# Kernel optimization log

Hardware: AMD Instinct MI355X
Metric: run time of the kernel (lower is better)

## Reference

```python
import jax, jax.numpy as jnp
import numpy as np


def hard_sigmoid(x):
    # Keras/Theano hard_sigmoid: clip(0.2*x + 0.5, 0, 1)
    return jnp.clip(0.2 * x + 0.5, 0.0, 1.0)


def _lstm_scan(x, Wi, Ui, bi, Wf, Uf, bf, Wc, Uc, bc, Wo, Uo, bo):
    # x: [B, T, D]. Precompute input-to-gate projections as big GEMMs -> [T, B, H]
    xi = jnp.einsum('btd,dh->tbh', x, Wi) + bi
    xf = jnp.einsum('btd,dh->tbh', x, Wf) + bf
    xc = jnp.einsum('btd,dh->tbh', x, Wc) + bc
    xo = jnp.einsum('btd,dh->tbh', x, Wo) + bo

    B = x.shape[0]
    H = Ui.shape[0]
    h0 = jnp.zeros((B, H), dtype=x.dtype)
    c0 = jnp.zeros((B, H), dtype=x.dtype)

    def step(carry, gates):
        h, c = carry
        gi, gf, go, gc = gates
        i_t = hard_sigmoid(gi + h @ Ui)
        f_t = hard_sigmoid(gf + h @ Uf)
        o_t = hard_sigmoid(go + h @ Uo)
        g_t = jnp.tanh(gc + h @ Uc)
        c_t = f_t * c + i_t * g_t
        h_t = o_t * jnp.tanh(c_t)
        return (h_t, c_t), h_t

    _, hs = jax.lax.scan(step, (h0, c0), (xi, xf, xo, xc))  # hs: [T, B, H]
    return hs.transpose(1, 0, 2)  # [B, T, H]


def _bidir_lstm(x,
                W_i, U_i, b_i, W_f, U_f, b_f, W_c, U_c, b_c, W_o, U_o, b_o,
                Wb_i, Ub_i, bb_i, Wb_f, Ub_f, bb_f, Wb_c, Ub_c, bb_c, Wb_o, Ub_o, bb_o):
    forward = _lstm_scan(x, W_i, U_i, b_i, W_f, U_f, b_f, W_c, U_c, b_c, W_o, U_o, b_o)
    # Theano scan(go_backwards=True) iterates the reversed sequence and stacks
    # outputs in iteration order WITHOUT re-reversing; replicate by flipping x
    # in time and not flipping the scan output back.
    backward = _lstm_scan(x[:, ::-1, :], Wb_i, Ub_i, bb_i, Wb_f, Ub_f, bb_f,
                          Wb_c, Ub_c, bb_c, Wb_o, Ub_o, bb_o)
    # output_mode == 'sum', return_sequences == True
    return forward + backward  # [B, T, H]


def setup_inputs() -> dict:
    B, T, D, H = 32, 512, 512, 512
    key = jax.random.key(0)
    keys = jax.random.split(key, 17)
    x = jax.random.normal(keys[0], (B, T, D), dtype=jnp.float32)
    s_w = 1.0 / np.sqrt(D)   # glorot-ish for input weights
    s_u = 1.0 / np.sqrt(H)   # orthogonal-ish scale for recurrent weights
    names = ['W_i', 'W_f', 'W_c', 'W_o', 'Wb_i', 'Wb_f', 'Wb_c', 'Wb_o']
    unames = ['U_i', 'U_f', 'U_c', 'U_o', 'Ub_i', 'Ub_f', 'Ub_c', 'Ub_o']
    inp = {'x': x}
    for j, n in enumerate(names):
        inp[n] = jax.random.normal(keys[1 + j], (D, H), dtype=jnp.float32) * s_w
    for j, n in enumerate(unames):
        inp[n] = jax.random.normal(keys[9 + j], (H, H), dtype=jnp.float32) * s_u
    for n in ['b_i', 'b_f', 'b_c', 'b_o', 'bb_i', 'bb_f', 'bb_c', 'bb_o']:
        inp[n] = jnp.zeros((H,), dtype=jnp.float32)
    return inp


def reference(x,
              W_i, U_i, b_i, W_f, U_f, b_f, W_c, U_c, b_c, W_o, U_o, b_o,
              Wb_i, Ub_i, bb_i, Wb_f, Ub_f, bb_f, Wb_c, Ub_c, bb_c, Wb_o, Ub_o, bb_o):
    return _bidir_lstm(x,
                       W_i, U_i, b_i, W_f, U_f, b_f, W_c, U_c, b_c, W_o, U_o, b_o,
                       Wb_i, Ub_i, bb_i, Wb_f, Ub_f, bb_f, Wb_c, Ub_c, bb_c,
                       Wb_o, Ub_o, bb_o)
```

## Files before the change

kernel.cpp:

```cpp
#include <hip/hip_runtime.h>

typedef _Float16 half8 __attribute__((ext_vector_type(8)));
typedef float f32x4 __attribute__((ext_vector_type(4)));

#define TT 512
#define HH 512

#define OFF_HPK   16777216
#define OFF_FLAGS 50331648
#define OFF_UPK   50339840
#define OFF_WPK   54534144

struct BiasPtrs { const float* b[8]; };

struct PackParams {
  const float* U[8];
  const float* W[8];
  _Float16* Upk;
  _Float16* Wpk;
};

__global__ void convert_x_kernel(const float* __restrict__ x, _Float16* __restrict__ x16) {
  const size_t i = ((size_t)blockIdx.x * blockDim.x + threadIdx.x) * 8;
  float4 v0 = *(const float4*)(x + i);
  float4 v1 = *(const float4*)(x + i + 4);
  half8 h;
  h[0] = (_Float16)v0.x; h[1] = (_Float16)v0.y; h[2] = (_Float16)v0.z; h[3] = (_Float16)v0.w;
  h[4] = (_Float16)v1.x; h[5] = (_Float16)v1.y; h[6] = (_Float16)v1.z; h[7] = (_Float16)v1.w;
  *(half8*)(x16 + i) = h;
}

__global__ void pack_frags_kernel(PackParams p) {
  const unsigned n = blockIdx.x * 256 + threadIdx.x;
  const unsigned o = n & 2097151u;
  const int sel = n >> 21;
  const int jj = o & 7, l = (o >> 3) & 63, kt = (o >> 9) & 15;
  const int ct = (o >> 13) & 1, j = (o >> 14) & 63, d = (o >> 20) & 1;
  const int r15 = l & 15, kg = l >> 4;
  const int g = r15 & 3;
  const int u = j * 8 + ct * 4 + (r15 >> 2);
  const int k = kt * 32 + kg * 8 + jj;
  const float* M = sel ? p.W[4 * d + g] : p.U[4 * d + g];
  _Float16* dst = sel ? p.Wpk : p.Upk;
  dst[o] = (_Float16)M[k * HH + u];
}

__global__ void zero_flags_kernel(int* __restrict__ p) {
  __hip_atomic_store(p + blockIdx.x * 256 + threadIdx.x, 0,
                     __ATOMIC_RELAXED, __HIP_MEMORY_SCOPE_AGENT);
}

__device__ __forceinline__ float hsig(float x) {
  return fminf(fmaxf(fmaf(x, 0.2f, 0.5f), 0.0f), 1.0f);
}

__device__ __forceinline__ float fast_tanh(float x) {
  const float e = __expf(2.0f * x);
  return fmaf(-2.0f, __builtin_amdgcn_rcpf(e + 1.0f), 1.0f);
}

__global__ __launch_bounds__(256, 1) void lstm_scan_kernel(
    const _Float16* __restrict__ x16,
    _Float16* __restrict__ h_pk,
    int* __restrict__ flags,
    const _Float16* __restrict__ Upk,
    const _Float16* __restrict__ Wpk,
    BiasPtrs bp) {
  const int tid = threadIdx.x;
  const int bid = blockIdx.x;
  const int d   = bid & 1;
  const int j   = bid >> 1;
  const int w   = tid >> 6;
  const int l   = tid & 63;
  const int r15 = l & 15;
  const int kg  = l >> 4;
  const int rt  = w & 1;
  const int ct  = w >> 1;
  const int arow = rt * 16 + r15;

  __shared__ __align__(16) half8 ulds[2 * 16 * 64];
  __shared__ __align__(16) half8 wlds[2 * 16 * 64];
  __shared__ __align__(16) float zlds[32 * 36];
  __shared__ __align__(16) unsigned short hlds[256];

  {
    const half8* ub = (const half8*)Upk;
    const half8* wb = (const half8*)Wpk;
    const int base = (((d * 64 + j) * 2 + ct) * 16) * 64 + l;
    if (rt == 0) {
#pragma unroll
      for (int kt = 0; kt < 16; ++kt) {
        ulds[(ct * 16 + kt) * 64 + l] = ub[base + kt * 64];
        wlds[(ct * 16 + kt) * 64 + l] = wb[base + kt * 64];
      }
    }
  }

  const int b_e  = tid >> 3;
  const int uu_e = tid & 7;
  const int u_e  = j * 8 + uu_e;
  const int slot_e = (uu_e >> 2) * 16 + (uu_e & 3) * 4;
  f32x4 biasv;
#pragma unroll
  for (int g = 0; g < 4; ++g) biasv[g] = bp.b[4 * d + g][u_e];

  __syncthreads();

  float c = 0.0f;

  for (int s = 0; s < TT; ++s) {
    const int t = d ? (TT - 1 - s) : s;

    half8 xa[16];
    {
      const half8* xb = (const half8*)(x16 + ((size_t)arow * TT + t) * HH);
#pragma unroll
      for (int kt = 0; kt < 16; ++kt) xa[kt] = xb[kt * 4 + kg];
    }
    __builtin_amdgcn_sched_barrier(0);

    if (s > 0) {
      if (tid < 64) {
        const int* fl = flags + ((d * 8 + ((s - 1) & 7)) << 6) + tid;
        while (__hip_atomic_load(fl, __ATOMIC_RELAXED, __HIP_MEMORY_SCOPE_AGENT) < s) {
          __builtin_amdgcn_s_sleep(1);
        }
      }
      __syncthreads();
    }
    __builtin_amdgcn_sched_barrier(0);

    half8 ha[16];
    if (s > 0) {
      const half8* hb = (const half8*)(h_pk + (size_t)(d * TT + (s - 1)) * 16384);
#pragma unroll
      for (int kt = 0; kt < 16; ++kt) ha[kt] = hb[(kt * 4 + kg) * 32 + arow];
    }
    __builtin_amdgcn_sched_barrier(0);

    f32x4 acc0 = {0,0,0,0}, acc1 = {0,0,0,0}, acc2 = {0,0,0,0}, acc3 = {0,0,0,0};
#pragma unroll
    for (int kt = 0; kt < 16; ++kt) {
      const half8 wk = wlds[(ct * 16 + kt) * 64 + l];
      if ((kt & 3) == 0)      acc0 = __builtin_amdgcn_mfma_f32_16x16x32_f16(xa[kt], wk, acc0, 0, 0, 0);
      else if ((kt & 3) == 1) acc1 = __builtin_amdgcn_mfma_f32_16x16x32_f16(xa[kt], wk, acc1, 0, 0, 0);
      else if ((kt & 3) == 2) acc2 = __builtin_amdgcn_mfma_f32_16x16x32_f16(xa[kt], wk, acc2, 0, 0, 0);
      else                    acc3 = __builtin_amdgcn_mfma_f32_16x16x32_f16(xa[kt], wk, acc3, 0, 0, 0);
    }
    __builtin_amdgcn_sched_barrier(0);

    if (s > 0) {
#pragma unroll
      for (int kt = 0; kt < 16; ++kt) {
        const half8 uk = ulds[(ct * 16 + kt) * 64 + l];
        if ((kt & 3) == 0)      acc0 = __builtin_amdgcn_mfma_f32_16x16x32_f16(ha[kt], uk, acc0, 0, 0, 0);
        else if ((kt & 3) == 1) acc1 = __builtin_amdgcn_mfma_f32_16x16x32_f16(ha[kt], uk, acc1, 0, 0, 0);
        else if ((kt & 3) == 2) acc2 = __builtin_amdgcn_mfma_f32_16x16x32_f16(ha[kt], uk, acc2, 0, 0, 0);
        else                    acc3 = __builtin_amdgcn_mfma_f32_16x16x32_f16(ha[kt], uk, acc3, 0, 0, 0);
      }
    }
    const f32x4 z = (acc0 + acc1) + (acc2 + acc3);

#pragma unroll
    for (int i = 0; i < 4; ++i)
      zlds[(rt * 16 + kg * 4 + i) * 36 + ct * 16 + r15] = z[i];
    __syncthreads();

    f32x4 pre = *(const f32x4*)&zlds[(size_t)b_e * 36 + slot_e] + biasv;
    const float ig = hsig(pre[0]);
    const float fg = hsig(pre[1]);
    const float gg = fast_tanh(pre[2]);
    const float og = hsig(pre[3]);
    c = fg * c + ig * gg;
    const float h = og * fast_tanh(c);

    hlds[tid] = __builtin_bit_cast(unsigned short, (_Float16)h);
    __syncthreads();

    if (tid < 64) {
      const unsigned long long v = ((const unsigned long long*)hlds)[tid];
      unsigned long long* dst = (unsigned long long*)h_pk +
                                ((size_t)(d * TT + s) * 64 + j) * 64 + tid;
      __hip_atomic_store(dst, v, __ATOMIC_RELAXED, __HIP_MEMORY_SCOPE_AGENT);
      asm volatile("s_waitcnt vmcnt(0)" ::: "memory");
      if (tid == 0)
        __hip_atomic_store(flags + ((d * 8 + (s & 7)) << 6) + j, s + 1,
                           __ATOMIC_RELAXED, __HIP_MEMORY_SCOPE_AGENT);
    }
  }
}

__global__ void sum_out_kernel(const _Float16* __restrict__ h_pk, float* __restrict__ out) {
  const unsigned idx = blockIdx.x * 256 + threadIdx.x;
  const int j = idx & 63;
  const int t = (idx >> 6) & 511;
  const int b = idx >> 15;
  half8 hf = ((const half8*)h_pk)[((size_t)t * 64 + j) * 32 + b];
  half8 hg = ((const half8*)h_pk)[((size_t)(TT + t) * 64 + j) * 32 + b];
  float* o = out + (((size_t)b * TT + t) * HH + j * 8);
  float4 r0, r1;
  r0.x = (float)hf[0] + (float)hg[0]; r0.y = (float)hf[1] + (float)hg[1];
  r0.z = (float)hf[2] + (float)hg[2]; r0.w = (float)hf[3] + (float)hg[3];
  r1.x = (float)hf[4] + (float)hg[4]; r1.y = (float)hf[5] + (float)hg[5];
  r1.z = (float)hf[6] + (float)hg[6]; r1.w = (float)hf[7] + (float)hg[7];
  *(float4*)o = r0;
  *(float4*)(o + 4) = r1;
}

extern "C" void kernel_launch(void* const* d_in, const int* in_sizes, int n_in,
                              void* d_out, int out_size, void* d_ws, size_t ws_size,
                              hipStream_t stream) {
  (void)in_sizes; (void)n_in; (void)out_size; (void)ws_size;
  char* ws = (char*)d_ws;
  _Float16* x16   = (_Float16*)ws;
  _Float16* h_pk  = (_Float16*)(ws + OFF_HPK);
  int*      flags = (int*)(ws + OFF_FLAGS);
  _Float16* Upk   = (_Float16*)(ws + OFF_UPK);
  _Float16* Wpk   = (_Float16*)(ws + OFF_WPK);

  convert_x_kernel<<<4096, 256, 0, stream>>>((const float*)d_in[0], x16);

  PackParams pp;
  for (int g = 0; g < 8; ++g) {
    pp.W[g] = (const float*)d_in[1 + g];
    pp.U[g] = (const float*)d_in[9 + g];
  }
  pp.Upk = Upk; pp.Wpk = Wpk;
  pack_frags_kernel<<<16384, 256, 0, stream>>>(pp);

  zero_flags_kernel<<<4, 256, 0, stream>>>(flags);

  BiasPtrs bp;
  for (int g = 0; g < 8; ++g) bp.b[g] = (const float*)d_in[17 + g];

  void* args[] = { (void*)&x16, (void*)&h_pk, (void*)&flags,
                   (void*)&Upk, (void*)&Wpk, (void*)&bp };
  hipLaunchCooperativeKernel((const void*)lstm_scan_kernel, dim3(128), dim3(256),
                             args, 0, stream);

  sum_out_kernel<<<4096, 256, 0, stream>>>(h_pk, (float*)d_out);
}
```

Baseline: 1.828 ms.

## Poison h buffer to drop store-wait before flag publish in LSTM scan

```diff
diff --git a/kernel.cpp b/kernel.cpp
--- a/kernel.cpp
+++ b/kernel.cpp
@@ -2,9 +2,11 @@
 
 typedef _Float16 half8 __attribute__((ext_vector_type(8)));
 typedef float f32x4 __attribute__((ext_vector_type(4)));
+typedef unsigned int u32x4 __attribute__((ext_vector_type(4)));
 
 #define TT 512
 #define HH 512
+#define P32 0xFFFFFFFFu
 
 #define OFF_HPK   16777216
 #define OFF_FLAGS 50331648
@@ -43,6 +45,14 @@
   const float* M = sel ? p.W[4 * d + g] : p.U[4 * d + g];
   _Float16* dst = sel ? p.Wpk : p.Upk;
   dst[o] = (_Float16)M[k * HH + u];
+}
+
+__global__ void poison_kernel(unsigned long long* __restrict__ p) {
+  const unsigned i = (blockIdx.x * 256 + threadIdx.x) * 4;
+#pragma unroll
+  for (int k = 0; k < 4; ++k)
+    __hip_atomic_store(p + i + k, 0xFFFFFFFFFFFFFFFFull,
+                       __ATOMIC_RELAXED, __HIP_MEMORY_SCOPE_AGENT);
 }
 
 __global__ void zero_flags_kernel(int* __restrict__ p) {
@@ -130,11 +140,12 @@
     }
     __builtin_amdgcn_sched_barrier(0);
 
-    half8 ha[16];
+    u32x4 hv[16];
+    const u32x4* hb4 = (const u32x4*)(h_pk + (size_t)(d * TT + (s > 0 ? s - 1 : 0)) * 16384);
     if (s > 0) {
-      const half8* hb = (const half8*)(h_pk + (size_t)(d * TT + (s - 1)) * 16384);
-#pragma unroll
-      for (int kt = 0; kt < 16; ++kt) ha[kt] = hb[(kt * 4 + kg) * 32 + arow];
+#pragma unroll
+      for (int kt = 0; kt < 16; ++kt)
+        hv[kt] = __builtin_nontemporal_load(hb4 + (kt * 4 + kg) * 32 + arow);
     }
     __builtin_amdgcn_sched_barrier(0);
 
@@ -152,11 +163,20 @@
     if (s > 0) {
 #pragma unroll
       for (int kt = 0; kt < 16; ++kt) {
+        u32x4 v = hv[kt];
+        if (v[0] == P32 || v[1] == P32 || v[2] == P32 || v[3] == P32) {
+          const unsigned* q = (const unsigned*)(hb4 + (kt * 4 + kg) * 32 + arow);
+          while (v[0] == P32) v[0] = __hip_atomic_load(q + 0, __ATOMIC_RELAXED, __HIP_MEMORY_SCOPE_AGENT);
+          while (v[1] == P32) v[1] = __hip_atomic_load(q + 1, __ATOMIC_RELAXED, __HIP_MEMORY_SCOPE_AGENT);
+          while (v[2] == P32) v[2] = __hip_atomic_load(q + 2, __ATOMIC_RELAXED, __HIP_MEMORY_SCOPE_AGENT);
+          while (v[3] == P32) v[3] = __hip_atomic_load(q + 3, __ATOMIC_RELAXED, __HIP_MEMORY_SCOPE_AGENT);
+        }
+        const half8 a  = __builtin_bit_cast(half8, v);
         const half8 uk = ulds[(ct * 16 + kt) * 64 + l];
-        if ((kt & 3) == 0)      acc0 = __builtin_amdgcn_mfma_f32_16x16x32_f16(ha[kt], uk, acc0, 0, 0, 0);
-        else if ((kt & 3) == 1) acc1 = __builtin_amdgcn_mfma_f32_16x16x32_f16(ha[kt], uk, acc1, 0, 0, 0);
-        else if ((kt & 3) == 2) acc2 = __builtin_amdgcn_mfma_f32_16x16x32_f16(ha[kt], uk, acc2, 0, 0, 0);
-        else                    acc3 = __builtin_amdgcn_mfma_f32_16x16x32_f16(ha[kt], uk, acc3, 0, 0, 0);
+        if ((kt & 3) == 0)      acc0 = __builtin_amdgcn_mfma_f32_16x16x32_f16(a, uk, acc0, 0, 0, 0);
+        else if ((kt & 3) == 1) acc1 = __builtin_amdgcn_mfma_f32_16x16x32_f16(a, uk, acc1, 0, 0, 0);
+        else if ((kt & 3) == 2) acc2 = __builtin_amdgcn_mfma_f32_16x16x32_f16(a, uk, acc2, 0, 0, 0);
+        else                    acc3 = __builtin_amdgcn_mfma_f32_16x16x32_f16(a, uk, acc3, 0, 0, 0);
       }
     }
     const f32x4 z = (acc0 + acc1) + (acc2 + acc3);
@@ -182,7 +202,6 @@
       unsigned long long* dst = (unsigned long long*)h_pk +
                                 ((size_t)(d * TT + s) * 64 + j) * 64 + tid;
       __hip_atomic_store(dst, v, __ATOMIC_RELAXED, __HIP_MEMORY_SCOPE_AGENT);
-      asm volatile("s_waitcnt vmcnt(0)" ::: "memory");
       if (tid == 0)
         __hip_atomic_store(flags + ((d * 8 + (s & 7)) << 6) + j, s + 1,
                            __ATOMIC_RELAXED, __HIP_MEMORY_SCOPE_AGENT);
@@ -228,6 +247,8 @@
   pp.Upk = Upk; pp.Wpk = Wpk;
   pack_frags_kernel<<<16384, 256, 0, stream>>>(pp);
 
+  poison_kernel<<<4096, 256, 0, stream>>>((unsigned long long*)(ws + OFF_HPK));
+
   zero_flags_kernel<<<4, 256, 0, stream>>>(flags);
 
   BiasPtrs bp;
```

New measurement: 2.506 ms. 37.1% more time.
